# Optimization experiments

Hardware: AMD Instinct MI355X
Metric: run time of the kernel (lower is better)

## Reference

```python
import jax, jax.numpy as jnp
import numpy as np

ETA = 0.01
EPSILON = 1e-08


def setup_inputs() -> dict:
    key = jax.random.key(0)
    k1, k2 = jax.random.split(key)
    B, N = 2000000, 16  # batch (time steps), num_assets
    weights = jax.random.uniform(k1, (B, N), dtype=jnp.float32)
    next_returns = jax.random.normal(k2, (B, N), dtype=jnp.float32) * 0.02
    return {"weights": weights, "next_returns": next_returns}


def reference(weights, next_returns):
    # portfolio return per time step: (B,)
    R = jnp.sum(weights * next_returns, axis=1)
    batch_size = R.shape[0]
    eta = jnp.asarray(ETA, R.dtype)
    eps = jnp.asarray(EPSILON, R.dtype)

    def step(carry, R_t):
        A_prev, B_prev = carry
        delta_A = eta * (R_t - A_prev)
        delta_B = eta * (R_t * R_t - B_prev)
        variance = jnp.maximum(B_prev - A_prev * A_prev, eps)
        denom = variance ** 1.5
        D_t = (B_prev * delta_A - 0.5 * A_prev * delta_B) / denom
        return (A_prev + delta_A, B_prev + delta_B), D_t

    init = (jnp.asarray(0.0, R.dtype), jnp.asarray(EPSILON, R.dtype))
    _, D = jax.lax.scan(step, init, R)
    return -jnp.sum(D) / batch_size
```

## Files before the change

### kernel.cpp

```cpp
#include <hip/hip_runtime.h>


#define D_ETA 0.01
#define D_C   (1.0 - D_ETA)
#define D_EPS 1e-8

constexpr int BLOCK = 256;
constexpr int K1_ROWS = 256;
constexpr int CHUNK = 2048;
constexpr int LPT   = CHUNK / BLOCK;

__device__ __forceinline__ float row_R(const float* __restrict__ w,
                                       const float* __restrict__ x,
                                       long long row) {
    const float4* w4 = (const float4*)(w + row * 16);
    const float4* x4 = (const float4*)(x + row * 16);
    double r = 0.0;
#pragma unroll
    for (int q = 0; q < 4; ++q) {
        float4 a = w4[q];
        float4 b = x4[q];
        r += (double)a.x * (double)b.x;
        r += (double)a.y * (double)b.y;
        r += (double)a.z * (double)b.z;
        r += (double)a.w * (double)b.w;
    }
    return (float)r;
}

__global__ __launch_bounds__(BLOCK) void k1_dots(
    const float* __restrict__ w, const float* __restrict__ x, int nrows,
    float* __restrict__ R)
{
    int tid = threadIdx.x;
    int q    = tid & 3;
    int rsub = tid >> 2;
    long long base = (long long)blockIdx.x * K1_ROWS;
    const float4* w4 = (const float4*)w;
    const float4* x4 = (const float4*)x;
#pragma unroll
    for (int it = 0; it < K1_ROWS / 64; ++it) {
        long long row = base + (long long)it * 64 + rsub;
        if (row < nrows) {
            long long f = row * 4 + q;
            float4 a = w4[f];
            float4 b = x4[f];
            double p = (double)a.x * (double)b.x
                     + (double)a.y * (double)b.y
                     + (double)a.z * (double)b.z
                     + (double)a.w * (double)b.w;
            p += __shfl_xor(p, 1, 64);
            p += __shfl_xor(p, 2, 64);
            if (q == 0) R[row] = (float)p;
        }
    }
}

__device__ __forceinline__ void block_scan(double& m, double& sA, double& sB,
                                           double* mS, double* aS, double* bS) {
    int tid = threadIdx.x;
    mS[tid] = m; aS[tid] = sA; bS[tid] = sB;
    __syncthreads();
#pragma unroll
    for (int off = 1; off < BLOCK; off <<= 1) {
        double pm = 1.0, pa = 0.0, pb = 0.0;
        if (tid >= off) { pm = mS[tid - off]; pa = aS[tid - off]; pb = bS[tid - off]; }
        __syncthreads();
        if (tid >= off) {
            sA = m * pa + sA;
            sB = m * pb + sB;
            m  = pm * m;
        }
        mS[tid] = m; aS[tid] = sA; bS[tid] = sB;
        __syncthreads();
    }
}

__device__ __forceinline__ int load_seg(const float* __restrict__ Rws,
                                        const float* __restrict__ w,
                                        const float* __restrict__ x,
                                        long long g0, int nrows, float* rv) {
    long long rem = (long long)nrows - g0;
    int len = rem >= LPT ? LPT : (rem > 0 ? (int)rem : 0);
    if (Rws) {
        if (len == LPT) {
            const float4* Rp = (const float4*)(Rws + g0);
            float4 u = Rp[0], v = Rp[1];
            rv[0]=u.x; rv[1]=u.y; rv[2]=u.z; rv[3]=u.w;
            rv[4]=v.x; rv[5]=v.y; rv[6]=v.z; rv[7]=v.w;
        } else {
            for (int k = 0; k < len; ++k) rv[k] = Rws[g0 + k];
        }
    } else {
        for (int k = 0; k < len; ++k) rv[k] = row_R(w, x, g0 + k);
    }
    return len;
}

__global__ __launch_bounds__(BLOCK) void k2_partials(
    const float* __restrict__ Rws,
    const float* __restrict__ w, const float* __restrict__ x, int nrows,
    double* __restrict__ blkM, double* __restrict__ blkA, double* __restrict__ blkB)
{
    __shared__ double mS[BLOCK], aS[BLOCK], bS[BLOCK];
    int tid = threadIdx.x;
    long long g0 = (long long)blockIdx.x * CHUNK + (long long)tid * LPT;
    float rv[LPT];
    int len = load_seg(Rws, w, x, g0, nrows, rv);

    double m = 1.0, sA = 0.0, sB = 0.0;
    for (int k = 0; k < len; ++k) {
        double r = (double)rv[k];
        sA = D_C * sA + D_ETA * r;
        sB = D_C * sB + D_ETA * (r * r);
        m *= D_C;
    }
    block_scan(m, sA, sB, mS, aS, bS);
    if (tid == BLOCK - 1) {
        blkM[blockIdx.x] = m;
        blkA[blockIdx.x] = sA;
        blkB[blockIdx.x] = sB;
    }
}

__global__ __launch_bounds__(BLOCK) void k3_scan(
    int nb,
    const double* __restrict__ blkM, const double* __restrict__ blkA,
    const double* __restrict__ blkB,
    double* __restrict__ A0, double* __restrict__ B0)
{
    __shared__ double mS[BLOCK], aS[BLOCK], bS[BLOCK];
    int tid = threadIdx.x;
    int K = (nb + BLOCK - 1) / BLOCK;
    int g0 = tid * K;
    int g1 = g0 + K; if (g1 > nb) g1 = nb;

    double m = 1.0, sA = 0.0, sB = 0.0;
    for (int g = g0; g < g1; ++g) {
        double mg = blkM[g], ag = blkA[g], bg = blkB[g];
        sA = mg * sA + ag;
        sB = mg * sB + bg;
        m *= mg;
    }
    block_scan(m, sA, sB, mS, aS, bS);

    double em = 1.0, ea = 0.0, eb = 0.0;
    if (tid > 0) { em = mS[tid - 1]; ea = aS[tid - 1]; eb = bS[tid - 1]; }
    double A = ea;
    double B = em * D_EPS + eb;
    for (int g = g0; g < g1; ++g) {
        A0[g] = A; B0[g] = B;
        double mg = blkM[g], ag = blkA[g], bg = blkB[g];
        A = mg * A + ag;
        B = mg * B + bg;
    }
}

__global__ __launch_bounds__(BLOCK) void k4_dsum(
    const float* __restrict__ Rws,
    const float* __restrict__ w, const float* __restrict__ x, int nrows,
    const double* __restrict__ A0, const double* __restrict__ B0,
    double* __restrict__ bsum)
{
    __shared__ double mS[BLOCK], aS[BLOCK], bS[BLOCK];
    __shared__ double wsum[BLOCK / 64];
    int tid = threadIdx.x;
    long long g0 = (long long)blockIdx.x * CHUNK + (long long)tid * LPT;
    float rv[LPT];
    int len = load_seg(Rws, w, x, g0, nrows, rv);

    double m = 1.0, sA = 0.0, sB = 0.0;
    for (int k = 0; k < len; ++k) {
        double r = (double)rv[k];
        sA = D_C * sA + D_ETA * r;
        sB = D_C * sB + D_ETA * (r * r);
        m *= D_C;
    }
    block_scan(m, sA, sB, mS, aS, bS);

    double em = 1.0, ea = 0.0, eb = 0.0;
    if (tid > 0) { em = mS[tid - 1]; ea = aS[tid - 1]; eb = bS[tid - 1]; }
    double A = em * A0[blockIdx.x] + ea;
    double B = em * B0[blockIdx.x] + eb;

    double dsum = 0.0;
    for (int k = 0; k < len; ++k) {
        double r = (double)rv[k];
        double dA = D_ETA * (r - A);
        double dB = D_ETA * (r * r - B);
        double var = B - A * A;
        if (var < D_EPS) var = D_EPS;
        double denom = var * sqrt(var);
        dsum += (B * dA - 0.5 * A * dB) / denom;
        A += dA;
        B += dB;
    }

#pragma unroll
    for (int off = 32; off > 0; off >>= 1) dsum += __shfl_down(dsum, off, 64);
    if ((tid & 63) == 0) wsum[tid >> 6] = dsum;
    __syncthreads();
    if (tid == 0) bsum[blockIdx.x] = wsum[0] + wsum[1] + wsum[2] + wsum[3];
}

__global__ __launch_bounds__(BLOCK) void k5_final(
    const double* __restrict__ bsum, int nb, int nrows, float* __restrict__ out)
{
    __shared__ double sh[BLOCK / 64];
    int tid = threadIdx.x;
    double s = 0.0;
    for (int i = tid; i < nb; i += BLOCK) s += bsum[i];
#pragma unroll
    for (int off = 32; off > 0; off >>= 1) s += __shfl_down(s, off, 64);
    if ((tid & 63) == 0) sh[tid >> 6] = s;
    __syncthreads();
    if (tid == 0) out[0] = (float)(-(sh[0] + sh[1] + sh[2] + sh[3]) / (double)nrows);
}

extern "C" void kernel_launch(void* const* d_in, const int* in_sizes, int n_in,
                              void* d_out, int out_size, void* d_ws, size_t ws_size,
                              hipStream_t stream)
{
    const float* w = (const float*)d_in[0];
    const float* x = (const float*)d_in[1];
    int nrows = in_sizes[0] / 16;
    int nb  = (nrows + CHUNK - 1) / CHUNK;
    int nb1 = (nrows + K1_ROWS - 1) / K1_ROWS;

    char* ws = (char*)d_ws;
    double* blkM = (double*)(ws + 64);
    double* blkA = blkM + nb;
    double* blkB = blkA + nb;
    double* A0   = blkB + nb;
    double* B0   = A0 + nb;
    double* bsum = B0 + nb;
    size_t off = 64 + (size_t)6 * nb * sizeof(double);
    off = (off + 255) & ~(size_t)255;
    float* Rws = nullptr;
    if (ws_size >= off + (size_t)nrows * sizeof(float))
        Rws = (float*)(ws + off);

    if (Rws)
        k1_dots<<<nb1, BLOCK, 0, stream>>>(w, x, nrows, Rws);
    k2_partials<<<nb, BLOCK, 0, stream>>>(Rws, w, x, nrows, blkM, blkA, blkB);
    k3_scan<<<1, BLOCK, 0, stream>>>(nb, blkM, blkA, blkB, A0, B0);
    k4_dsum<<<nb, BLOCK, 0, stream>>>(Rws, w, x, nrows, A0, B0, bsum);
    k5_final<<<1, BLOCK, 0, stream>>>(bsum, nb, nrows, (float*)d_out);
}
```

Measured before the change: 286.5 us.

## Fuse row dot products with per-chunk scan aggregation and shrink chunk size

Merges the row dot-product kernel with the per-chunk affine-scan partial kernel. Each block computes its dot products into shared memory, writes them to the workspace, and scans them locally, which removes one kernel launch and one pass over the R array. Each block now issues eight float4 loads per thread up front to get more memory-level parallelism. CHUNK shrinks from 2048 to 512, so there are four times as many blocks and two rows per thread in the later pass. The cost is a longer serial loop in the single-block carry scan.

```diff
diff --git a/kernel.cpp b/kernel.cpp
--- a/kernel.cpp
+++ b/kernel.cpp
@@ -6,8 +6,8 @@
 #define D_EPS 1e-8
 
 constexpr int BLOCK = 256;
-constexpr int K1_ROWS = 256;
-constexpr int CHUNK = 2048;
+constexpr int K1_IT = 8;
+constexpr int CHUNK = K1_IT * 64;
 constexpr int LPT   = CHUNK / BLOCK;
 
 __device__ __forceinline__ float row_R(const float* __restrict__ w,
@@ -28,32 +28,9 @@
     return (float)r;
 }
 
-__global__ __launch_bounds__(BLOCK) void k1_dots(
-    const float* __restrict__ w, const float* __restrict__ x, int nrows,
-    float* __restrict__ R)
-{
-    int tid = threadIdx.x;
-    int q    = tid & 3;
-    int rsub = tid >> 2;
-    long long base = (long long)blockIdx.x * K1_ROWS;
-    const float4* w4 = (const float4*)w;
-    const float4* x4 = (const float4*)x;
-#pragma unroll
-    for (int it = 0; it < K1_ROWS / 64; ++it) {
-        long long row = base + (long long)it * 64 + rsub;
-        if (row < nrows) {
-            long long f = row * 4 + q;
-            float4 a = w4[f];
-            float4 b = x4[f];
-            double p = (double)a.x * (double)b.x
-                     + (double)a.y * (double)b.y
-                     + (double)a.z * (double)b.z
-                     + (double)a.w * (double)b.w;
-            p += __shfl_xor(p, 1, 64);
-            p += __shfl_xor(p, 2, 64);
-            if (q == 0) R[row] = (float)p;
-        }
-    }
+__device__ __forceinline__ double dot4d(float4 a, float4 b) {
+    return (double)a.x * (double)b.x + (double)a.y * (double)b.y
+         + (double)a.z * (double)b.z + (double)a.w * (double)b.w;
 }
 
 __device__ __forceinline__ void block_scan(double& m, double& sA, double& sB,
@@ -76,41 +53,93 @@
     }
 }
 
-__device__ __forceinline__ int load_seg(const float* __restrict__ Rws,
-                                        const float* __restrict__ w,
-                                        const float* __restrict__ x,
-                                        long long g0, int nrows, float* rv) {
+__global__ __launch_bounds__(BLOCK) void k1_dots_agg(
+    const float* __restrict__ w, const float* __restrict__ x, int nrows,
+    float* __restrict__ R,
+    double* __restrict__ blkM, double* __restrict__ blkA, double* __restrict__ blkB)
+{
+    __shared__ float Rs[CHUNK];
+    __shared__ double mS[BLOCK], aS[BLOCK], bS[BLOCK];
+    int tid = threadIdx.x;
+    int q    = tid & 3;
+    int rsub = tid >> 2;
+    long long base = (long long)blockIdx.x * CHUNK;
+    const float4* w4 = (const float4*)w;
+    const float4* x4 = (const float4*)x;
+    long long f0 = base * 4 + tid;
+
+    double p[K1_IT];
+    if (base + CHUNK <= (long long)nrows) {
+        float4 a[K1_IT], b[K1_IT];
+#pragma unroll
+        for (int it = 0; it < K1_IT; ++it) a[it] = w4[f0 + it * 256];
+#pragma unroll
+        for (int it = 0; it < K1_IT; ++it) b[it] = x4[f0 + it * 256];
+#pragma unroll
+        for (int it = 0; it < K1_IT; ++it) p[it] = dot4d(a[it], b[it]);
+    } else {
+#pragma unroll
+        for (int it = 0; it < K1_IT; ++it) {
+            long long row = base + it * 64 + rsub;
+            p[it] = 0.0;
+            if (row < nrows) {
+                float4 a = w4[row * 4 + q];
+                float4 b = x4[row * 4 + q];
+                p[it] = dot4d(a, b);
+            }
+        }
+    }
+
+#pragma unroll
+    for (int it = 0; it < K1_IT; ++it) {
+        p[it] += __shfl_xor(p[it], 1, 64);
+        p[it] += __shfl_xor(p[it], 2, 64);
+    }
+
+    if (q == 0) {
+#pragma unroll
+        for (int it = 0; it < K1_IT; ++it) {
+            long long row = base + it * 64 + rsub;
+            float rf = (float)p[it];
+            Rs[it * 64 + rsub] = rf;
+            if (row < nrows) R[row] = rf;
+        }
+    }
+    __syncthreads();
+
+    int start = tid * LPT;
+    long long g = base + start;
+    long long rem = (long long)nrows - g;
+    int len = rem >= LPT ? LPT : (rem > 0 ? (int)rem : 0);
+
+    double m = 1.0, sA = 0.0, sB = 0.0;
+    for (int k = 0; k < len; ++k) {
+        double r = (double)Rs[start + k];
+        sA = D_C * sA + D_ETA * r;
+        sB = D_C * sB + D_ETA * (r * r);
+        m *= D_C;
+    }
+    block_scan(m, sA, sB, mS, aS, bS);
+    if (tid == BLOCK - 1) {
+        blkM[blockIdx.x] = m;
+        blkA[blockIdx.x] = sA;
+        blkB[blockIdx.x] = sB;
+    }
+}
+
+__global__ __launch_bounds__(BLOCK) void k2_partials_fb(
+    const float* __restrict__ w, const float* __restrict__ x, int nrows,
+    double* __restrict__ blkM, double* __restrict__ blkA, double* __restrict__ blkB)
+{
+    __shared__ double mS[BLOCK], aS[BLOCK], bS[BLOCK];
+    int tid = threadIdx.x;
+    long long g0 = (long long)blockIdx.x * CHUNK + (long long)tid * LPT;
     long long rem = (long long)nrows - g0;
     int len = rem >= LPT ? LPT : (rem > 0 ? (int)rem : 0);
-    if (Rws) {
-        if (len == LPT) {
-            const float4* Rp = (const float4*)(Rws + g0);
-            float4 u = Rp[0], v = Rp[1];
-            rv[0]=u.x; rv[1]=u.y; rv[2]=u.z; rv[3]=u.w;
-            rv[4]=v.x; rv[5]=v.y; rv[6]=v.z; rv[7]=v.w;
-        } else {
-            for (int k = 0; k < len; ++k) rv[k] = Rws[g0 + k];
-        }
-    } else {
-        for (int k = 0; k < len; ++k) rv[k] = row_R(w, x, g0 + k);
-    }
-    return len;
-}
-
-__global__ __launch_bounds__(BLOCK) void k2_partials(
-    const float* __restrict__ Rws,
-    const float* __restrict__ w, const float* __restrict__ x, int nrows,
-    double* __restrict__ blkM, double* __restrict__ blkA, double* __restrict__ blkB)
-{
-    __shared__ double mS[BLOCK], aS[BLOCK], bS[BLOCK];
-    int tid = threadIdx.x;
-    long long g0 = (long long)blockIdx.x * CHUNK + (long long)tid * LPT;
-    float rv[LPT];
-    int len = load_seg(Rws, w, x, g0, nrows, rv);
-
-    double m = 1.0, sA = 0.0, sB = 0.0;
-    for (int k = 0; k < len; ++k) {
-        double r = (double)rv[k];
+
+    double m = 1.0, sA = 0.0, sB = 0.0;
+    for (int k = 0; k < len; ++k) {
+        double r = (double)row_R(w, x, g0 + k);
         sA = D_C * sA + D_ETA * r;
         sB = D_C * sB + D_ETA * (r * r);
         m *= D_C;
@@ -166,8 +195,20 @@
     __shared__ double wsum[BLOCK / 64];
     int tid = threadIdx.x;
     long long g0 = (long long)blockIdx.x * CHUNK + (long long)tid * LPT;
+    long long rem = (long long)nrows - g0;
+    int len = rem >= LPT ? LPT : (rem > 0 ? (int)rem : 0);
+
     float rv[LPT];
-    int len = load_seg(Rws, w, x, g0, nrows, rv);
+    if (Rws) {
+        if (len == LPT) {
+            float2 u = *(const float2*)(Rws + g0);
+            rv[0] = u.x; rv[1] = u.y;
+        } else {
+            for (int k = 0; k < len; ++k) rv[k] = Rws[g0 + k];
+        }
+    } else {
+        for (int k = 0; k < len; ++k) rv[k] = row_R(w, x, g0 + k);
+    }
 
     double m = 1.0, sA = 0.0, sB = 0.0;
     for (int k = 0; k < len; ++k) {
@@ -224,8 +265,7 @@
     const float* w = (const float*)d_in[0];
     const float* x = (const float*)d_in[1];
     int nrows = in_sizes[0] / 16;
-    int nb  = (nrows + CHUNK - 1) / CHUNK;
-    int nb1 = (nrows + K1_ROWS - 1) / K1_ROWS;
+    int nb = (nrows + CHUNK - 1) / CHUNK;
 
     char* ws = (char*)d_ws;
     double* blkM = (double*)(ws + 64);
@@ -240,9 +280,11 @@
     if (ws_size >= off + (size_t)nrows * sizeof(float))
         Rws = (float*)(ws + off);
 
-    if (Rws)
-        k1_dots<<<nb1, BLOCK, 0, stream>>>(w, x, nrows, Rws);
-    k2_partials<<<nb, BLOCK, 0, stream>>>(Rws, w, x, nrows, blkM, blkA, blkB);
+    if (Rws) {
+        k1_dots_agg<<<nb, BLOCK, 0, stream>>>(w, x, nrows, Rws, blkM, blkA, blkB);
+    } else {
+        k2_partials_fb<<<nb, BLOCK, 0, stream>>>(w, x, nrows, blkM, blkA, blkB);
+    }
     k3_scan<<<1, BLOCK, 0, stream>>>(nb, blkM, blkA, blkB, A0, B0);
     k4_dsum<<<nb, BLOCK, 0, stream>>>(Rws, w, x, nrows, A0, B0, bsum);
     k5_final<<<1, BLOCK, 0, stream>>>(bsum, nb, nrows, (float*)d_out);
```

Measured after the change: 309.7 us. 8.1% more time.
